# Performance work log

Measured on AMD Instinct MI355X. Metric: run time of the kernel, lower is better.

The kernel has to match this reference:

```python
import jax, jax.numpy as jnp
import numpy as np
import math

HEAD_DIM = 64

def setup_inputs() -> dict:
    key = jax.random.key(0)
    kq, kk, kv = jax.random.split(key, 3)
    B, H, S, D = 2, 16, 2048, HEAD_DIM
    Q = jax.random.normal(kq, (B, H, S, D), dtype=jnp.float32)
    K = jax.random.normal(kk, (B, H, S, D), dtype=jnp.float32)
    V = jax.random.normal(kv, (B, H, S, D), dtype=jnp.float32)
    mask = jnp.ones((B, S), dtype=jnp.float32)
    return {"Q": Q, "K": K, "V": V, "mask": mask}

def reference(Q, K, V, mask):
    # dot: [B, H, S, S]
    dot = jnp.einsum('bhqd,bhkd->bhqk', Q, K) / math.sqrt(HEAD_DIM)
    # additive mask: -1e6 where mask == 0 (mask broadcast over heads and query dim)
    dot = dot - 1000000.0 * (1.0 - mask[:, None, None, :])
    attn = jax.nn.softmax(dot, axis=-1)
    # dropout_prob = 0 -> identity
    X = jnp.einsum('bhqk,bhkd->bhqd', attn, V)
    return X
```

## Files before the change

kernel.cpp:

```cpp
#include <hip/hip_runtime.h>
#include <hip/hip_bf16.h>
#include <hip/hip_fp16.h>
#include <stdint.h>


#define S_LEN   2048
#define DHEAD   64
#define QTILE   64
#define KTILE   64
#define NTILE   (S_LEN / KTILE)
#define LDK     72
#define CEXP    9.0f
#define SCL2E   0.18033688011112042f
#define L2E     1.4426950408889634f

typedef __attribute__((ext_vector_type(4))) float    f32x4;
typedef __attribute__((ext_vector_type(2))) _Float16 f16x2;
typedef __attribute__((ext_vector_type(4))) _Float16 f16x4;
typedef __attribute__((ext_vector_type(8))) _Float16 f16x8;

static __device__ __forceinline__ float exp2_fast(float x) {
#if __has_builtin(__builtin_amdgcn_exp2f)
  return __builtin_amdgcn_exp2f(x);
#else
  float r;
  asm("v_exp_f32 %0, %1" : "=v"(r) : "v"(x));
  return r;
#endif
}

static __device__ __forceinline__ f16x2 pk(float a, float b) {
  auto r = __builtin_amdgcn_cvt_pkrtz(a, b);
  union { decltype(r) i; f16x2 o; } u;
  u.i = r;
  return u.o;
}

__global__ __launch_bounds__(256, 4) void attn_fwd(
    const float* __restrict__ Q, const float* __restrict__ K,
    const float* __restrict__ V, const float* __restrict__ Mk,
    float* __restrict__ O) {
  __shared__ _Float16 kls[2][KTILE * LDK];
  __shared__ _Float16 vls[2][DHEAD * LDK];
  __shared__ float    madd[2][KTILE];

  const int tid  = threadIdx.x;
  const int lane = tid & 63;
  const int wave = tid >> 6;
  const int quad = lane >> 4;
  const int l16  = lane & 15;

  const int blk  = blockIdx.x;
  const int bh   = (blk & 7) | (((blk >> 3) & 3) << 3);
  const int qblk = blk >> 5;
  const int b    = bh >> 4;

  const size_t base = (size_t)bh * S_LEN * DHEAD;
  const float* Qb = Q + base;
  const float* Kb = K + base;
  const float* Vb = V + base;
  const float* Mb = Mk + (size_t)b * S_LEN;
  float* Ob = O + base;

  const int q = qblk * QTILE + wave * 16 + l16;
  f16x8 qf[2];
  {
    const float* qp = Qb + (size_t)q * DHEAD + quad * 8;
#pragma unroll
    for (int kb = 0; kb < 2; ++kb) {
      float4 a = *(const float4*)(qp + kb * 32);
      float4 c = *(const float4*)(qp + kb * 32 + 4);
      union { f16x2 h[4]; f16x8 v; } r;
      r.h[0] = pk(a.x * SCL2E, a.y * SCL2E);
      r.h[1] = pk(a.z * SCL2E, a.w * SCL2E);
      r.h[2] = pk(c.x * SCL2E, c.y * SCL2E);
      r.h[3] = pk(c.z * SCL2E, c.w * SCL2E);
      qf[kb] = r.v;
    }
  }

  f32x4 xacc[4] = {{0.f,0.f,0.f,0.f},{0.f,0.f,0.f,0.f},
                   {0.f,0.f,0.f,0.f},{0.f,0.f,0.f,0.f}};
  float l_lane = 0.0f;

  const int krow = tid >> 2;
  const int kcol = (tid & 3) * 16;
  const int vkv  = (tid >> 4) * 4;
  const int vd   = (tid & 15) * 4;
  const int gsw  = ((tid >> 4) ^ (tid & 15)) * 4;

  auto load_tile = [&](int j0, float4* kreg, float4* vreg, float& mreg) {
    const float* kp = Kb + (size_t)(j0 + krow) * DHEAD + kcol;
#pragma unroll
    for (int i = 0; i < 4; ++i) kreg[i] = *(const float4*)(kp + 4 * i);
    const float* vp = Vb + (size_t)(j0 + vkv) * DHEAD + vd;
#pragma unroll
    for (int r = 0; r < 4; ++r) vreg[r] = *(const float4*)(vp + r * DHEAD);
    mreg = (tid < KTILE) ? Mb[j0 + tid] : 0.0f;
  };
  auto store_tile = [&](int bi, const float4* kreg, const float4* vreg,
                        float mreg) {
#pragma unroll
    for (int i = 0; i < 4; ++i) {
      union { f16x2 h[2]; f16x4 v; } r;
      r.h[0] = pk(kreg[i].x, kreg[i].y);
      r.h[1] = pk(kreg[i].z, kreg[i].w);
      *(f16x4*)(&kls[bi][krow * LDK + kcol + 4 * i]) = r.v;
    }
    union { f16x2 h[2]; f16x4 v; } t0, t1, t2, t3;
    t0.h[0] = pk(vreg[0].x, vreg[1].x); t0.h[1] = pk(vreg[2].x, vreg[3].x);
    t1.h[0] = pk(vreg[0].y, vreg[1].y); t1.h[1] = pk(vreg[2].y, vreg[3].y);
    t2.h[0] = pk(vreg[0].z, vreg[1].z); t2.h[1] = pk(vreg[2].z, vreg[3].z);
    t3.h[0] = pk(vreg[0].w, vreg[1].w); t3.h[1] = pk(vreg[2].w, vreg[3].w);
    *(f16x4*)(&vls[bi][(vd + 0) * LDK + gsw]) = t0.v;
    *(f16x4*)(&vls[bi][(vd + 1) * LDK + gsw]) = t1.v;
    *(f16x4*)(&vls[bi][(vd + 2) * LDK + gsw]) = t2.v;
    *(f16x4*)(&vls[bi][(vd + 3) * LDK + gsw]) = t3.v;
    if (tid < KTILE)
      madd[bi][tid] = -CEXP - (1.0e6f * L2E) * (1.0f - mreg);
  };

  {
    float4 kreg[4], vreg[4]; float mreg;
    load_tile(0, kreg, vreg, mreg);
    store_tile(0, kreg, vreg, mreg);
  }
  __syncthreads();

  for (int jt = 0; jt < NTILE; ++jt) {
    const int cur = jt & 1;
    const int nxt = cur ^ 1;
    float4 kreg[4], vreg[4]; float mreg = 0.0f;
    const bool more = (jt + 1 < NTILE);
    if (more) load_tile((jt + 1) * KTILE, kreg, vreg, mreg);

    f16x4 pf[4];
#pragma unroll
    for (int t = 0; t < 4; ++t) {
      const _Float16* kr = &kls[cur][(t * 16 + l16) * LDK + quad * 8];
      f16x8 ka0 = *(const f16x8*)(kr);
      f16x8 ka1 = *(const f16x8*)(kr + 32);
      f32x4 st = *(const f32x4*)(&madd[cur][t * 16 + quad * 4]);
      st = __builtin_amdgcn_mfma_f32_16x16x32_f16(ka0, qf[0], st, 0, 0, 0);
      st = __builtin_amdgcn_mfma_f32_16x16x32_f16(ka1, qf[1], st, 0, 0, 0);
      float p0 = exp2_fast(st.x);
      float p1 = exp2_fast(st.y);
      float p2 = exp2_fast(st.z);
      float p3 = exp2_fast(st.w);
      l_lane += (p0 + p1) + (p2 + p3);
      union { f16x2 h[2]; f16x4 v; } r;
      r.h[0] = pk(p0, p1);
      r.h[1] = pk(p2, p3);
      pf[t] = r.v;
    }
#pragma unroll
    for (int m = 0; m < 4; ++m) {
      f32x4 x = xacc[m];
      const int rowb = (m * 16 + l16) * LDK;
      const int swb  = 4 * m + (l16 >> 2);
#pragma unroll
      for (int t = 0; t < 4; ++t) {
        f16x4 vf = *(const f16x4*)(&vls[cur][rowb + 4 * ((4 * t + quad) ^ swb)]);
        x = __builtin_amdgcn_mfma_f32_16x16x16f16(vf, pf[t], x, 0, 0, 0);
      }
      xacc[m] = x;
    }

    if (more) store_tile(nxt, kreg, vreg, mreg);
    __syncthreads();
  }

  float l = l_lane;
  l += __shfl_xor(l, 16, 64);
  l += __shfl_xor(l, 32, 64);
  const float rl = 1.0f / l;
  float* op = Ob + (size_t)q * DHEAD;
#pragma unroll
  for (int m = 0; m < 4; ++m) {
    float4 o;
    o.x = xacc[m].x * rl;
    o.y = xacc[m].y * rl;
    o.z = xacc[m].z * rl;
    o.w = xacc[m].w * rl;
    *(float4*)(op + m * 16 + quad * 4) = o;
  }
}

extern "C" void kernel_launch(void* const* d_in, const int* in_sizes, int n_in,
                              void* d_out, int out_size, void* d_ws, size_t ws_size,
                              hipStream_t stream) {
  const float* Q = (const float*)d_in[0];
  const float* K = (const float*)d_in[1];
  const float* V = (const float*)d_in[2];
  const float* M = (const float*)d_in[3];
  float* O = (float*)d_out;
  hipLaunchKernelGGL(attn_fwd, dim3(1024), dim3(256), 0, stream, Q, K, V, M, O);
}
```

Baseline: 147.5 us.

## Pre-convert K/V to fp16 in workspace and stream tiles via global_load_lds

Adds two prep kernels that convert K and V to fp16 once per call: K in a pre-swizzled layout, V in a pre-transposed layout, plus a precomputed mask-additive array. The attention kernel then fills LDS with direct global-to-LDS 16-byte loads, with no register staging and no per-block fp32 conversion. This removes the redundant K/V conversion that each of the 32 query blocks per head repeated, and halves the bytes the attention kernel reads for K/V. In exchange it adds two extra launches and a workspace round trip. A fallback kernel with a new V LDS swizzle runs when the workspace is too small.

```diff
diff --git a/kernel.cpp b/kernel.cpp
--- a/kernel.cpp
+++ b/kernel.cpp
@@ -1,14 +1,11 @@
 #include <hip/hip_runtime.h>
-#include <hip/hip_bf16.h>
 #include <hip/hip_fp16.h>
 #include <stdint.h>
 
 
 #define S_LEN   2048
 #define DHEAD   64
-#define QTILE   64
-#define KTILE   64
-#define NTILE   (S_LEN / KTILE)
+#define NTILE   32
 #define LDK     72
 #define CEXP    9.0f
 #define SCL2E   0.18033688011112042f
@@ -36,19 +33,55 @@
   return u.o;
 }
 
-__global__ __launch_bounds__(256, 4) void attn_fwd(
-    const float* __restrict__ Q, const float* __restrict__ K,
-    const float* __restrict__ V, const float* __restrict__ Mk,
+#define GLDS16(g, l)                                                  \
+  __builtin_amdgcn_global_load_lds(                                   \
+      (const __attribute__((address_space(1))) void*)(g),             \
+      (__attribute__((address_space(3))) void*)(l), 16, 0, 0)
+
+__global__ __launch_bounds__(256) void prep_k(
+    const float* __restrict__ K, const float* __restrict__ Mk,
+    _Float16* __restrict__ Kswz, float* __restrict__ madd_g) {
+  const int idx = blockIdx.x * 256 + threadIdx.x;
+  const int c  = idx & 7;
+  const int kv = (idx >> 3) & 2047;
+  const int bh = idx >> 14;
+  const float* src = K + ((size_t)bh * S_LEN + kv) * DHEAD + c * 8;
+  float4 a = *(const float4*)(src);
+  float4 d = *(const float4*)(src + 4);
+  union { f16x2 h[4]; f16x8 v; } r;
+  r.h[0] = pk(a.x, a.y); r.h[1] = pk(a.z, a.w);
+  r.h[2] = pk(d.x, d.y); r.h[3] = pk(d.z, d.w);
+  *(f16x8*)(Kswz + ((size_t)bh * S_LEN + kv) * DHEAD + ((c + kv) & 7) * 8) = r.v;
+  if (idx < 2 * S_LEN)
+    madd_g[idx] = -CEXP - (1.0e6f * L2E) * (1.0f - Mk[idx]);
+}
+
+__global__ __launch_bounds__(256) void prep_v(
+    const float* __restrict__ V, _Float16* __restrict__ Vg) {
+  const int idx = blockIdx.x * 256 + threadIdx.x;
+  const int d  = idx & 63;
+  const int g  = (idx >> 6) & 15;
+  const int j  = (idx >> 10) & 31;
+  const int bh = idx >> 15;
+  const float* src = V + ((size_t)bh * S_LEN + j * 64 + g * 4) * DHEAD + d;
+  float v0 = src[0], v1 = src[64], v2 = src[128], v3 = src[192];
+  union { f16x2 h[2]; f16x4 v; } r;
+  r.h[0] = pk(v0, v1); r.h[1] = pk(v2, v3);
+  *(f16x4*)(Vg + (size_t)idx * 4) = r.v;
+}
+
+__global__ __launch_bounds__(256, 4) void attn_ws(
+    const float* __restrict__ Q, const _Float16* __restrict__ Kswz,
+    const _Float16* __restrict__ Vg, const float* __restrict__ madd_g,
     float* __restrict__ O) {
-  __shared__ _Float16 kls[2][KTILE * LDK];
-  __shared__ _Float16 vls[2][DHEAD * LDK];
-  __shared__ float    madd[2][KTILE];
+  __shared__ __align__(16) _Float16 kls[2][4096];
+  __shared__ __align__(16) _Float16 vls[2][4096];
 
   const int tid  = threadIdx.x;
   const int lane = tid & 63;
   const int wave = tid >> 6;
   const int quad = lane >> 4;
-  const int l16  = lane & 15;
+  const int x    = lane & 15;
 
   const int blk  = blockIdx.x;
   const int bh   = (blk & 7) | (((blk >> 3) & 3) << 3);
@@ -56,13 +89,13 @@
   const int b    = bh >> 4;
 
   const size_t base = (size_t)bh * S_LEN * DHEAD;
-  const float* Qb = Q + base;
-  const float* Kb = K + base;
-  const float* Vb = V + base;
-  const float* Mb = Mk + (size_t)b * S_LEN;
+  const float*    Qb = Q + base;
+  const _Float16* Kb = Kswz + base;
+  const _Float16* Vb = Vg + base;
+  const float*    Mb = madd_g + b * S_LEN;
   float* Ob = O + base;
 
-  const int q = qblk * QTILE + wave * 16 + l16;
+  const int q = qblk * 64 + wave * 16 + x;
   f16x8 qf[2];
   {
     const float* qp = Qb + (size_t)q * DHEAD + quad * 8;
@@ -79,6 +112,118 @@
     }
   }
 
+  auto prefetch = [&](int j, int bi) {
+    const _Float16* ks = Kb + j * 4096 + tid * 8;
+    const _Float16* vs = Vb + j * 4096 + tid * 8;
+    GLDS16(ks,        &kls[bi][tid * 8]);
+    GLDS16(ks + 2048, &kls[bi][tid * 8 + 2048]);
+    GLDS16(vs,        &vls[bi][tid * 8]);
+    GLDS16(vs + 2048, &vls[bi][tid * 8 + 2048]);
+  };
+
+  f32x4 xacc[4] = {{0.f,0.f,0.f,0.f},{0.f,0.f,0.f,0.f},
+                   {0.f,0.f,0.f,0.f},{0.f,0.f,0.f,0.f}};
+  float l_lane = 0.0f;
+
+  prefetch(0, 0);
+  __syncthreads();
+
+  for (int jt = 0; jt < NTILE; ++jt) {
+    const int cur = jt & 1;
+    if (jt + 1 < NTILE) prefetch(jt + 1, cur ^ 1);
+
+    const _Float16* k0 = &kls[cur][x * 64 + ((quad + x) & 7) * 8];
+    const _Float16* k1 = &kls[cur][x * 64 + ((quad + 4 + x) & 7) * 8];
+    const float*    mp = Mb + jt * 64 + quad * 4;
+    f16x4 pf[4];
+#pragma unroll
+    for (int t = 0; t < 4; ++t) {
+      f16x8 ka0 = *(const f16x8*)(k0 + t * 1024);
+      f16x8 ka1 = *(const f16x8*)(k1 + t * 1024);
+      f32x4 st = *(const f32x4*)(mp + t * 16);
+      st = __builtin_amdgcn_mfma_f32_16x16x32_f16(ka0, qf[0], st, 0, 0, 0);
+      st = __builtin_amdgcn_mfma_f32_16x16x32_f16(ka1, qf[1], st, 0, 0, 0);
+      float p0 = exp2_fast(st.x);
+      float p1 = exp2_fast(st.y);
+      float p2 = exp2_fast(st.z);
+      float p3 = exp2_fast(st.w);
+      l_lane += (p0 + p1) + (p2 + p3);
+      union { f16x2 h[2]; f16x4 v; } r;
+      r.h[0] = pk(p0, p1);
+      r.h[1] = pk(p2, p3);
+      pf[t] = r.v;
+    }
+    const _Float16* vbase = &vls[cur][256 * quad + 4 * x];
+#pragma unroll
+    for (int m = 0; m < 4; ++m) {
+      f32x4 xa = xacc[m];
+#pragma unroll
+      for (int t = 0; t < 4; ++t) {
+        f16x4 vf = *(const f16x4*)(vbase + 1024 * t + 64 * m);
+        xa = __builtin_amdgcn_mfma_f32_16x16x16f16(vf, pf[t], xa, 0, 0, 0);
+      }
+      xacc[m] = xa;
+    }
+    __syncthreads();
+  }
+
+  float l = l_lane;
+  l += __shfl_xor(l, 16, 64);
+  l += __shfl_xor(l, 32, 64);
+  const float rl = 1.0f / l;
+  float* op = Ob + (size_t)q * DHEAD;
+#pragma unroll
+  for (int m = 0; m < 4; ++m) {
+    float4 o;
+    o.x = xacc[m].x * rl; o.y = xacc[m].y * rl;
+    o.z = xacc[m].z * rl; o.w = xacc[m].w * rl;
+    *(float4*)(op + m * 16 + quad * 4) = o;
+  }
+}
+
+__global__ __launch_bounds__(256, 4) void attn_fb(
+    const float* __restrict__ Q, const float* __restrict__ K,
+    const float* __restrict__ V, const float* __restrict__ Mk,
+    float* __restrict__ O) {
+  __shared__ __align__(16) _Float16 kls[2][64 * LDK];
+  __shared__ __align__(16) _Float16 vls[2][4096];
+  __shared__ float madd[2][64];
+
+  const int tid  = threadIdx.x;
+  const int lane = tid & 63;
+  const int wave = tid >> 6;
+  const int quad = lane >> 4;
+  const int l16  = lane & 15;
+
+  const int blk  = blockIdx.x;
+  const int bh   = (blk & 7) | (((blk >> 3) & 3) << 3);
+  const int qblk = blk >> 5;
+  const int b    = bh >> 4;
+
+  const size_t base = (size_t)bh * S_LEN * DHEAD;
+  const float* Qb = Q + base;
+  const float* Kb = K + base;
+  const float* Vb = V + base;
+  const float* Mb = Mk + (size_t)b * S_LEN;
+  float* Ob = O + base;
+
+  const int q = qblk * 64 + wave * 16 + l16;
+  f16x8 qf[2];
+  {
+    const float* qp = Qb + (size_t)q * DHEAD + quad * 8;
+#pragma unroll
+    for (int kb = 0; kb < 2; ++kb) {
+      float4 a = *(const float4*)(qp + kb * 32);
+      float4 c = *(const float4*)(qp + kb * 32 + 4);
+      union { f16x2 h[4]; f16x8 v; } r;
+      r.h[0] = pk(a.x * SCL2E, a.y * SCL2E);
+      r.h[1] = pk(a.z * SCL2E, a.w * SCL2E);
+      r.h[2] = pk(c.x * SCL2E, c.y * SCL2E);
+      r.h[3] = pk(c.z * SCL2E, c.w * SCL2E);
+      qf[kb] = r.v;
+    }
+  }
+
   f32x4 xacc[4] = {{0.f,0.f,0.f,0.f},{0.f,0.f,0.f,0.f},
                    {0.f,0.f,0.f,0.f},{0.f,0.f,0.f,0.f}};
   float l_lane = 0.0f;
@@ -87,7 +232,8 @@
   const int kcol = (tid & 3) * 16;
   const int vkv  = (tid >> 4) * 4;
   const int vd   = (tid & 15) * 4;
-  const int gsw  = ((tid >> 4) ^ (tid & 15)) * 4;
+  const int xs   = tid & 15;
+  const int s    = tid >> 4;
 
   auto load_tile = [&](int j0, float4* kreg, float4* vreg, float& mreg) {
     const float* kp = Kb + (size_t)(j0 + krow) * DHEAD + kcol;
@@ -96,7 +242,7 @@
     const float* vp = Vb + (size_t)(j0 + vkv) * DHEAD + vd;
 #pragma unroll
     for (int r = 0; r < 4; ++r) vreg[r] = *(const float4*)(vp + r * DHEAD);
-    mreg = (tid < KTILE) ? Mb[j0 + tid] : 0.0f;
+    mreg = (tid < 64) ? Mb[j0 + tid] : 0.0f;
   };
   auto store_tile = [&](int bi, const float4* kreg, const float4* vreg,
                         float mreg) {
@@ -112,11 +258,13 @@
     t1.h[0] = pk(vreg[0].y, vreg[1].y); t1.h[1] = pk(vreg[2].y, vreg[3].y);
     t2.h[0] = pk(vreg[0].z, vreg[1].z); t2.h[1] = pk(vreg[2].z, vreg[3].z);
     t3.h[0] = pk(vreg[0].w, vreg[1].w); t3.h[1] = pk(vreg[2].w, vreg[3].w);
-    *(f16x4*)(&vls[bi][(vd + 0) * LDK + gsw]) = t0.v;
-    *(f16x4*)(&vls[bi][(vd + 1) * LDK + gsw]) = t1.v;
-    *(f16x4*)(&vls[bi][(vd + 2) * LDK + gsw]) = t2.v;
-    *(f16x4*)(&vls[bi][(vd + 3) * LDK + gsw]) = t3.v;
-    if (tid < KTILE)
+    const int wb = (xs & 3) + 16 * s;
+    const int xh = xs >> 2;
+    *(f16x4*)(&vls[bi][4 * (wb + 4 * (xh ^ 0) + 256 * 0)]) = t0.v;
+    *(f16x4*)(&vls[bi][4 * (wb + 4 * (xh ^ 1) + 256 * 1)]) = t1.v;
+    *(f16x4*)(&vls[bi][4 * (wb + 4 * (xh ^ 2) + 256 * 2)]) = t2.v;
+    *(f16x4*)(&vls[bi][4 * (wb + 4 * (xh ^ 3) + 256 * 3)]) = t3.v;
+    if (tid < 64)
       madd[bi][tid] = -CEXP - (1.0e6f * L2E) * (1.0f - mreg);
   };
 
@@ -132,7 +280,7 @@
     const int nxt = cur ^ 1;
     float4 kreg[4], vreg[4]; float mreg = 0.0f;
     const bool more = (jt + 1 < NTILE);
-    if (more) load_tile((jt + 1) * KTILE, kreg, vreg, mreg);
+    if (more) load_tile((jt + 1) * 64, kreg, vreg, mreg);
 
     f16x4 pf[4];
 #pragma unroll
@@ -155,15 +303,15 @@
     }
 #pragma unroll
     for (int m = 0; m < 4; ++m) {
-      f32x4 x = xacc[m];
-      const int rowb = (m * 16 + l16) * LDK;
-      const int swb  = 4 * m + (l16 >> 2);
+      f32x4 xa = xacc[m];
+      const int rb = 4 * ((l16 >> 2) + 4 * (m ^ (l16 & 3)) + 16 * quad +
+                          256 * (l16 & 3));
 #pragma unroll
       for (int t = 0; t < 4; ++t) {
-        f16x4 vf = *(const f16x4*)(&vls[cur][rowb + 4 * ((4 * t + quad) ^ swb)]);
-        x = __builtin_amdgcn_mfma_f32_16x16x16f16(vf, pf[t], x, 0, 0, 0);
+        f16x4 vf = *(const f16x4*)(&vls[cur][rb + 256 * t]);
+        xa = __builtin_amdgcn_mfma_f32_16x16x16f16(vf, pf[t], xa, 0, 0, 0);
       }
-      xacc[m] = x;
+      xacc[m] = xa;
     }
 
     if (more) store_tile(nxt, kreg, vreg, mreg);
@@ -178,10 +326,8 @@
 #pragma unroll
   for (int m = 0; m < 4; ++m) {
     float4 o;
-    o.x = xacc[m].x * rl;
-    o.y = xacc[m].y * rl;
-    o.z = xacc[m].z * rl;
-    o.w = xacc[m].w * rl;
+    o.x = xacc[m].x * rl; o.y = xacc[m].y * rl;
+    o.z = xacc[m].z * rl; o.w = xacc[m].w * rl;
     *(float4*)(op + m * 16 + quad * 4) = o;
   }
 }
@@ -194,5 +340,16 @@
   const float* V = (const float*)d_in[2];
   const float* M = (const float*)d_in[3];
   float* O = (float*)d_out;
-  hipLaunchKernelGGL(attn_fwd, dim3(1024), dim3(256), 0, stream, Q, K, V, M, O);
-}
+
+  const size_t need = 16777216 + 2 * S_LEN * sizeof(float);
+  if (ws_size >= need) {
+    _Float16* Kswz = (_Float16*)d_ws;
+    _Float16* Vg   = Kswz + 4194304;
+    float*    madd = (float*)((char*)d_ws + 16777216);
+    hipLaunchKernelGGL(prep_k, dim3(2048), dim3(256), 0, stream, K, M, Kswz, madd);
+    hipLaunchKernelGGL(prep_v, dim3(4096), dim3(256), 0, stream, V, Vg);
+    hipLaunchKernelGGL(attn_ws, dim3(1024), dim3(256), 0, stream, Q, Kswz, Vg, madd, O);
+  } else {
+    hipLaunchKernelGGL(attn_fb, dim3(1024), dim3(256), 0, stream, Q, K, V, M, O);
+  }
+}
```

After: 149.5 us. No clear change (+1.4%).
